# Kernel optimization log

Measured on AMD Instinct MI355X. Metric: run time of the kernel, lower is better.

## Reference

```python
import jax, jax.numpy as jnp
import numpy as np

B, S, DM, H, HD = 2, 4096, 768, 12, 64   # longformer-base-4096
W = 256    # one-sided attention window (attention_window=512)
NB = S // W
G = 16     # number of leading global-attention tokens ([CLS]+query)
OUT = 512  # hidden_dim of final fc


def setup_inputs() -> dict:
    key = jax.random.key(0)
    ks = jax.random.split(key, 11)
    def w(k, shape):
        return jax.random.normal(k, shape, jnp.float32) * 0.02
    z = lambda n: jnp.zeros((n,), jnp.float32)
    return {
        "x": jax.random.normal(ks[0], (B, S, DM), jnp.float32),
        "wq": w(ks[1], (DM, DM)), "bq": z(DM),
        "wk": w(ks[2], (DM, DM)), "bk": z(DM),
        "wv": w(ks[3], (DM, DM)), "bv": z(DM),
        "wqg": w(ks[4], (DM, DM)), "bqg": z(DM),
        "wkg": w(ks[5], (DM, DM)), "bkg": z(DM),
        "wvg": w(ks[6], (DM, DM)), "bvg": z(DM),
        "wo": w(ks[7], (DM, DM)), "bo": z(DM),
        "wp": w(ks[8], (DM, DM)), "bp": z(DM),
        "wfc": w(ks[9], (DM, OUT)), "bfc": z(OUT),
    }


def _longformer_forward(x, wq, bq, wk, bk, wv, bv, wqg, bqg, wkg, bkg,
                        wvg, bvg, wo, bo, wp, bp, wfc, bfc):
    scale = jnp.float32(1.0 / np.sqrt(HD))
    q = ((x @ wq + bq) * scale).reshape(B, S, H, HD)
    k = (x @ wk + bk).reshape(B, S, H, HD)
    v = (x @ wv + bv).reshape(B, S, H, HD)

    # --- sliding-window (banded) attention via overlapping key/value blocks ---
    kp = jnp.pad(k, ((0, 0), (W, W), (0, 0), (0, 0)))  # [B, S+2W, H, HD]
    vp = jnp.pad(v, ((0, 0), (W, W), (0, 0), (0, 0)))
    blk = jnp.arange(NB)[:, None] * W + jnp.arange(3 * W)[None, :]  # [NB,3W]
    kb = kp[:, blk]  # [B, NB, 3W, H, HD]
    vb = vp[:, blk]
    qb = q.reshape(B, NB, W, H, HD)
    sc_loc = jnp.einsum('bnqhd,bnkhd->bhnqk', qb, kb)  # [B,H,NB,W,3W]

    i = jnp.arange(W)[:, None]
    j = jnp.arange(3 * W)[None, :]
    band = (j >= i) & (j <= i + 2 * W)                       # |rel| <= W
    abs_k = (jnp.arange(NB)[:, None, None] - 1) * W + j[None]  # [NB,W,3W]
    # mask padding, out-of-band, and global keys (handled separately per HF)
    valid = band[None] & (abs_k >= 0) & (abs_k < S) & (abs_k >= G)
    sc_loc = jnp.where(valid[None, None], sc_loc, jnp.float32(-1e9))

    # every query also attends to the G global keys (regular k/v per HF)
    sc_glb = jnp.einsum('bqhd,bghd->bhqg', q, k[:, :G])  # [B,H,S,G]

    sc = jnp.concatenate([sc_glb, sc_loc.reshape(B, H, S, 3 * W)], axis=-1)
    p = jax.nn.softmax(sc, axis=-1)
    p_g, p_l = p[..., :G], p[..., G:]
    out = jnp.einsum('bhqg,bghd->bqhd', p_g, v[:, :G])
    out = out + jnp.einsum('bhnqk,bnkhd->bnqhd',
                           p_l.reshape(B, H, NB, W, 3 * W), vb).reshape(B, S, H, HD)

    # --- global queries: full attention with the dedicated global projections ---
    qg = ((x[:, :G] @ wqg + bqg) * scale).reshape(B, G, H, HD)
    kg = (x @ wkg + bkg).reshape(B, S, H, HD)
    vg = (x @ wvg + bvg).reshape(B, S, H, HD)
    pg = jax.nn.softmax(jnp.einsum('bghd,bshd->bhgs', qg, kg), axis=-1)
    out_g = jnp.einsum('bhgs,bshd->bghd', pg, vg)
    out = jnp.concatenate([out_g, out[:, G:]], axis=1)

    attn = out.reshape(B, S, DM) @ wo + bo
    pooled = jnp.tanh(attn[:, 0] @ wp + bp)  # HF pooler on [CLS]
    return pooled @ wfc + bfc                # final nn.Linear -> [B, OUT]


def reference(x, wq, bq, wk, bk, wv, bv, wqg, bqg, wkg, bkg, wvg, bvg,
              wo, bo, wp, bp, wfc, bfc):
    return _longformer_forward(x, wq, bq, wk, bk, wv, bv, wqg, bqg, wkg,
                               bkg, wvg, bvg, wo, bo, wp, bp, wfc, bfc)
```

## Files before the change

kernel.cpp:

```cpp
#include <hip/hip_runtime.h>
#include <hip/hip_bf16.h>

#define BB 2
#define SS 4096
#define DM 768
#define NH 12
#define OUTC 512
#define QSCALE 0.125f
#define NCHUNK 128
#define CS 32
#define JT 32

__device__ __forceinline__ float wave_sum64(float v) {
#pragma unroll
  for (int o = 32; o > 0; o >>= 1) v += __shfl_xor(v, o, 64);
  return v;
}

__global__ __launch_bounds__(256) void kA(const float* __restrict__ x,
    const float* __restrict__ wqg, const float* __restrict__ bqg,
    const float* __restrict__ wkg, const float* __restrict__ bkg,
    float* __restrict__ qw_ws, float* __restrict__ qb_ws,
    float* __restrict__ l_ws, float* __restrict__ xw_ws) {
  int h = blockIdx.x, b = blockIdx.y, js = blockIdx.z, t = threadIdx.x;
  __shared__ float x0[DM];
  __shared__ float red[4][64];
  __shared__ float qg0[64];
  for (int i = t; i < DM; i += 256) x0[i] = x[(size_t)b*SS*DM + i];
  for (int i = t; i < 384; i += 256)
    xw_ws[((size_t)b*NH + h)*DM + js*384 + i] = 0.f;
  if (js == 0 && t == 0) l_ws[b*NH + h] = 0.f;
  __syncthreads();
  int d = t & 63, g = t >> 6;
  float p = 0.f;
  for (int j = g*192; j < g*192 + 192; ++j)
    p += x0[j] * wqg[(size_t)j*DM + h*64 + d];
  red[g][d] = p;
  __syncthreads();
  if (t < 64)
    qg0[t] = (red[0][t] + red[1][t] + red[2][t] + red[3][t] + bqg[h*64 + t]) * QSCALE;
  __syncthreads();
  if (js == 0 && t == 0) {
    float qb = 0.f;
    for (int dd = 0; dd < 64; ++dd) qb += qg0[dd] * bkg[h*64 + dd];
    qb_ws[b*NH + h] = qb;
  }
  const float4* qg4 = (const float4*)qg0;
  for (int jj = t; jj < 384; jj += 256) {
    int j = js*384 + jj;
    const float4* wr = (const float4*)(wkg + (size_t)j*DM + h*64);
    float acc = 0.f;
#pragma unroll
    for (int q = 0; q < 16; ++q) {
      float4 wv = wr[q], qv = qg4[q];
      acc += wv.x*qv.x + wv.y*qv.y + wv.z*qv.z + wv.w*qv.w;
    }
    qw_ws[((size_t)b*NH + h)*DM + j] = acc;
  }
}

__global__ __launch_bounds__(256) void kB(const float* __restrict__ x,
    const float* __restrict__ qw_ws, const float* __restrict__ qb_ws,
    float* __restrict__ l_ws, float* __restrict__ xw_ws) {
  int chunk = blockIdx.x, b = blockIdx.y;
  int t = threadIdx.x, lane = t & 63, w = t >> 6;
  __shared__ alignas(16) float qw[NH*DM];
  __shared__ float qb[NH];
  __shared__ alignas(16) float pl[CS*NH];
  for (int i = t; i < NH*DM; i += 256) qw[i] = qw_ws[(size_t)b*NH*DM + i];
  if (t < NH) qb[t] = qb_ws[b*NH + t];
  __syncthreads();
  const size_t xbase = ((size_t)b*SS + chunk*CS) * DM;
  const float4* x4 = (const float4*)(x + xbase);
  const float4* qw4 = (const float4*)qw;
  float lacc = 0.f;

  for (int batch = 0; batch < 2; ++batch) {
    int sl = w*8 + batch*4;
    float acc[4][NH];
#pragma unroll
    for (int si = 0; si < 4; ++si)
#pragma unroll
      for (int hh = 0; hh < NH; ++hh) acc[si][hh] = 0.f;
#pragma unroll
    for (int k = 0; k < 3; ++k) {
      int jq = k*64 + lane;
      float4 xf[4];
#pragma unroll
      for (int si = 0; si < 4; ++si)
        xf[si] = x4[(size_t)(sl + si)*192 + jq];
#pragma unroll
      for (int hh = 0; hh < NH; ++hh) {
        float4 qv = qw4[hh*192 + jq];
#pragma unroll
        for (int si = 0; si < 4; ++si)
          acc[si][hh] += xf[si].x*qv.x + xf[si].y*qv.y + xf[si].z*qv.z + xf[si].w*qv.w;
      }
    }
    float preg = 0.f;
#pragma unroll
    for (int si = 0; si < 4; ++si)
#pragma unroll
      for (int hh = 0; hh < NH; ++hh) {
        float r = wave_sum64(acc[si][hh]);
        float pp = __expf(r + qb[hh]);
        if (lane == hh) lacc += pp;
        if (lane == si*NH + hh) preg = pp;
      }
    if (lane < 4*NH) pl[(sl + lane/NH)*NH + (lane % NH)] = preg;
  }
  if (lane < NH) atomicAdd(&l_ws[b*NH + lane], lacc);
  __syncthreads();

  float a2[NH][3];
#pragma unroll
  for (int hh = 0; hh < NH; ++hh)
#pragma unroll
    for (int i = 0; i < 3; ++i) a2[hh][i] = 0.f;
  for (int s = 0; s < CS; ++s) {
    float4 p0 = *(const float4*)(&pl[s*NH + 0]);
    float4 p1 = *(const float4*)(&pl[s*NH + 4]);
    float4 p2 = *(const float4*)(&pl[s*NH + 8]);
    float pv[NH] = {p0.x,p0.y,p0.z,p0.w, p1.x,p1.y,p1.z,p1.w, p2.x,p2.y,p2.z,p2.w};
    float xv[3];
#pragma unroll
    for (int i = 0; i < 3; ++i)
      xv[i] = x[xbase + (size_t)s*DM + t + 256*i];
#pragma unroll
    for (int hh = 0; hh < NH; ++hh)
#pragma unroll
      for (int i = 0; i < 3; ++i) a2[hh][i] += pv[hh]*xv[i];
  }
#pragma unroll
  for (int hh = 0; hh < NH; ++hh)
#pragma unroll
    for (int i = 0; i < 3; ++i)
      atomicAdd(&xw_ws[((size_t)b*NH + hh)*DM + t + 256*i], a2[hh][i]);
}

__global__ __launch_bounds__(256) void kE1(const float* __restrict__ xw_ws,
    const float* __restrict__ l_ws, const float* __restrict__ wvg,
    const float* __restrict__ bvg, float* __restrict__ out0_ws,
    float* __restrict__ zbuf) {
  int h = blockIdx.x, b = blockIdx.y, t = threadIdx.x;
  __shared__ float xws[DM];
  __shared__ float red[4][64];
  int bid = b*NH + h;
  if (t < 128) zbuf[bid*128 + t] = 0.f;
  float inv = 1.f / l_ws[b*NH + h];
  for (int i = 0; i < 3; ++i) {
    int j = t + 256*i;
    xws[j] = xw_ws[((size_t)b*NH + h)*DM + j] * inv;
  }
  __syncthreads();
  int ci = t & 63, g = t >> 6;
  float acc = 0.f;
  for (int j = g*192; j < g*192 + 192; ++j)
    acc += xws[j] * wvg[(size_t)j*DM + h*64 + ci];
  red[g][ci] = acc;
  __syncthreads();
  if (t < 64)
    out0_ws[b*DM + h*64 + t] =
        red[0][t] + red[1][t] + red[2][t] + red[3][t] + bvg[h*64 + t];
}

__global__ __launch_bounds__(192) void kT(const float* __restrict__ inraw,
    const float* __restrict__ bias, const float* __restrict__ W,
    float* __restrict__ outacc) {
  int jb = blockIdx.x, t = threadIdx.x;
  __shared__ float xs[2][DM/JT];
  const int JR = DM/JT;
  int j0 = jb*JR;
  if (t < 2*JR) {
    int bb = t / JR, jj = t % JR;
    float v = inraw[bb*DM + j0 + jj];
    if (bias) v += bias[j0 + jj];
    xs[bb][jj] = v;
  }
  __syncthreads();
  float4 a0 = {0,0,0,0}, a1 = {0,0,0,0};
  const float4* W4 = (const float4*)W;
#pragma unroll 4
  for (int jj = 0; jj < JR; ++jj) {
    float4 wv = W4[(size_t)(j0 + jj)*192 + t];
    float s0 = xs[0][jj], s1 = xs[1][jj];
    a0.x += s0*wv.x; a0.y += s0*wv.y; a0.z += s0*wv.z; a0.w += s0*wv.w;
    a1.x += s1*wv.x; a1.y += s1*wv.y; a1.z += s1*wv.z; a1.w += s1*wv.w;
  }
  int c = t*4;
  atomicAdd(&outacc[c+0], a0.x); atomicAdd(&outacc[c+1], a0.y);
  atomicAdd(&outacc[c+2], a0.z); atomicAdd(&outacc[c+3], a0.w);
  atomicAdd(&outacc[DM+c+0], a1.x); atomicAdd(&outacc[DM+c+1], a1.y);
  atomicAdd(&outacc[DM+c+2], a1.z); atomicAdd(&outacc[DM+c+3], a1.w);
}

__global__ __launch_bounds__(256) void kT3(const float* __restrict__ pooledraw,
    const float* __restrict__ bp, const float* __restrict__ wfc,
    const float* __restrict__ bfc, float* __restrict__ out) {
  int tile = blockIdx.x, b = blockIdx.y, t = threadIdx.x;
  __shared__ float pl[DM];
  __shared__ float red[4][64];
  for (int i = t; i < DM; i += 256) pl[i] = tanhf(pooledraw[b*DM + i] + bp[i]);
  __syncthreads();
  int ci = t & 63, g = t >> 6;
  int c = tile*64 + ci;
  float acc = 0.f;
  for (int j = g*192; j < g*192 + 192; ++j)
    acc += pl[j] * wfc[(size_t)j*OUTC + c];
  red[g][ci] = acc;
  __syncthreads();
  if (t < 64)
    out[(size_t)b*OUTC + tile*64 + t] =
        red[0][t] + red[1][t] + red[2][t] + red[3][t] + bfc[tile*64 + t];
}

extern "C" void kernel_launch(void* const* d_in, const int* in_sizes, int n_in,
                              void* d_out, int out_size, void* d_ws, size_t ws_size,
                              hipStream_t stream) {
  const float* x   = (const float*)d_in[0];
  const float* wqg = (const float*)d_in[7];
  const float* bqg = (const float*)d_in[8];
  const float* wkg = (const float*)d_in[9];
  const float* bkg = (const float*)d_in[10];
  const float* wvg = (const float*)d_in[11];
  const float* bvg = (const float*)d_in[12];
  const float* wo  = (const float*)d_in[13];
  const float* bo  = (const float*)d_in[14];
  const float* wp  = (const float*)d_in[15];
  const float* bp  = (const float*)d_in[16];
  const float* wfc = (const float*)d_in[17];
  const float* bfc = (const float*)d_in[18];

  float* ws        = (float*)d_ws;
  float* qw        = ws;
  float* qb        = ws + 18432;
  float* l         = ws + 18456;
  float* xw        = ws + 18480;
  float* out0      = ws + 36912;
  float* attnraw   = ws + 38448;
  float* pooledraw = ws + 39984;

  kA <<<dim3(NH, BB, 2),  256, 0, stream>>>(x, wqg, bqg, wkg, bkg, qw, qb, l, xw);
  kB <<<dim3(NCHUNK, BB), 256, 0, stream>>>(x, qw, qb, l, xw);
  kE1<<<dim3(NH, BB),     256, 0, stream>>>(xw, l, wvg, bvg, out0, attnraw);
  kT <<<dim3(JT),         192, 0, stream>>>(out0, nullptr, wo, attnraw);
  kT <<<dim3(JT),         192, 0, stream>>>(attnraw, bo, wp, pooledraw);
  kT3<<<dim3(8, BB),      256, 0, stream>>>(pooledraw, bp, wfc, bfc, (float*)d_out);
}
```

Measured before the change: 199.7 us.

## Split kB across head groups and vectorize small GEMV kernels with float4

The main kernel kB is split into four head groups of three heads each along a new grid dimension, so it launches four times as many blocks, each using less shared memory and fewer registers. The cost is that x is re-read once per head group. kA splits the wkg projection four ways instead of two. kA, kE1 and kT3 switch their GEMVs to float4 weight loads with a 16-way reduction, and kT doubles its block count and fully unrolls its loop. Together these aim to raise occupancy and parallelism in a launch-bound, low-occupancy pipeline.

```diff
diff --git a/kernel.cpp b/kernel.cpp
--- a/kernel.cpp
+++ b/kernel.cpp
@@ -9,7 +9,12 @@
 #define QSCALE 0.125f
 #define NCHUNK 128
 #define CS 32
-#define JT 32
+#define HPB 3
+#define HG  (NH/HPB)
+#define JSA 4
+#define JWA (DM/JSA)
+#define JT 64
+#define JR (DM/JT)
 
 __device__ __forceinline__ float wave_sum64(float v) {
 #pragma unroll
@@ -24,30 +29,47 @@
     float* __restrict__ l_ws, float* __restrict__ xw_ws) {
   int h = blockIdx.x, b = blockIdx.y, js = blockIdx.z, t = threadIdx.x;
   __shared__ float x0[DM];
-  __shared__ float red[4][64];
+  __shared__ float4 red4[16][16];
   __shared__ float qg0[64];
   for (int i = t; i < DM; i += 256) x0[i] = x[(size_t)b*SS*DM + i];
-  for (int i = t; i < 384; i += 256)
-    xw_ws[((size_t)b*NH + h)*DM + js*384 + i] = 0.f;
+  for (int i = t; i < JWA; i += 256)
+    xw_ws[((size_t)b*NH + h)*DM + js*JWA + i] = 0.f;
   if (js == 0 && t == 0) l_ws[b*NH + h] = 0.f;
   __syncthreads();
-  int d = t & 63, g = t >> 6;
-  float p = 0.f;
-  for (int j = g*192; j < g*192 + 192; ++j)
-    p += x0[j] * wqg[(size_t)j*DM + h*64 + d];
-  red[g][d] = p;
-  __syncthreads();
-  if (t < 64)
-    qg0[t] = (red[0][t] + red[1][t] + red[2][t] + red[3][t] + bqg[h*64 + t]) * QSCALE;
-  __syncthreads();
-  if (js == 0 && t == 0) {
-    float qb = 0.f;
-    for (int dd = 0; dd < 64; ++dd) qb += qg0[dd] * bkg[h*64 + dd];
-    qb_ws[b*NH + h] = qb;
+  {
+    int cq = t & 15, jg = t >> 4;
+    const float4* wq4 = (const float4*)wqg;
+    float4 a = {0.f, 0.f, 0.f, 0.f};
+#pragma unroll 8
+    for (int jo = 0; jo < 48; ++jo) {
+      int j = jg*48 + jo;
+      float xv = x0[j];
+      float4 wv = wq4[(size_t)j*(DM/4) + h*16 + cq];
+      a.x += xv*wv.x; a.y += xv*wv.y; a.z += xv*wv.z; a.w += xv*wv.w;
+    }
+    red4[jg][cq] = a;
+  }
+  __syncthreads();
+  if (t < 16) {
+    float4 a = {0.f, 0.f, 0.f, 0.f};
+#pragma unroll
+    for (int jg = 0; jg < 16; ++jg) {
+      float4 r = red4[jg][t];
+      a.x += r.x; a.y += r.y; a.z += r.z; a.w += r.w;
+    }
+    float4 bq = ((const float4*)(bqg + h*64))[t];
+    a.x = (a.x + bq.x)*QSCALE; a.y = (a.y + bq.y)*QSCALE;
+    a.z = (a.z + bq.z)*QSCALE; a.w = (a.w + bq.w)*QSCALE;
+    ((float4*)qg0)[t] = a;
+  }
+  __syncthreads();
+  if (js == 0 && t < 64) {
+    float v = wave_sum64(qg0[t] * bkg[h*64 + t]);
+    if (t == 0) qb_ws[b*NH + h] = v;
   }
   const float4* qg4 = (const float4*)qg0;
-  for (int jj = t; jj < 384; jj += 256) {
-    int j = js*384 + jj;
+  for (int jj = t; jj < JWA; jj += 256) {
+    int j = js*JWA + jj;
     const float4* wr = (const float4*)(wkg + (size_t)j*DM + h*64);
     float acc = 0.f;
 #pragma unroll
@@ -62,13 +84,13 @@
 __global__ __launch_bounds__(256) void kB(const float* __restrict__ x,
     const float* __restrict__ qw_ws, const float* __restrict__ qb_ws,
     float* __restrict__ l_ws, float* __restrict__ xw_ws) {
-  int chunk = blockIdx.x, b = blockIdx.y;
+  int chunk = blockIdx.x, b = blockIdx.y, h0 = blockIdx.z * HPB;
   int t = threadIdx.x, lane = t & 63, w = t >> 6;
-  __shared__ alignas(16) float qw[NH*DM];
-  __shared__ float qb[NH];
-  __shared__ alignas(16) float pl[CS*NH];
-  for (int i = t; i < NH*DM; i += 256) qw[i] = qw_ws[(size_t)b*NH*DM + i];
-  if (t < NH) qb[t] = qb_ws[b*NH + t];
+  __shared__ alignas(16) float qw[HPB*DM];
+  __shared__ float qb[HPB];
+  __shared__ alignas(16) float pl[CS*HPB];
+  for (int i = t; i < HPB*DM; i += 256) qw[i] = qw_ws[((size_t)b*NH + h0)*DM + i];
+  if (t < HPB) qb[t] = qb_ws[b*NH + h0 + t];
   __syncthreads();
   const size_t xbase = ((size_t)b*SS + chunk*CS) * DM;
   const float4* x4 = (const float4*)(x + xbase);
@@ -77,11 +99,11 @@
 
   for (int batch = 0; batch < 2; ++batch) {
     int sl = w*8 + batch*4;
-    float acc[4][NH];
+    float acc[4][HPB];
 #pragma unroll
     for (int si = 0; si < 4; ++si)
 #pragma unroll
-      for (int hh = 0; hh < NH; ++hh) acc[si][hh] = 0.f;
+      for (int hh = 0; hh < HPB; ++hh) acc[si][hh] = 0.f;
 #pragma unroll
     for (int k = 0; k < 3; ++k) {
       int jq = k*64 + lane;
@@ -90,7 +112,7 @@
       for (int si = 0; si < 4; ++si)
         xf[si] = x4[(size_t)(sl + si)*192 + jq];
 #pragma unroll
-      for (int hh = 0; hh < NH; ++hh) {
+      for (int hh = 0; hh < HPB; ++hh) {
         float4 qv = qw4[hh*192 + jq];
 #pragma unroll
         for (int si = 0; si < 4; ++si)
@@ -101,41 +123,40 @@
 #pragma unroll
     for (int si = 0; si < 4; ++si)
 #pragma unroll
-      for (int hh = 0; hh < NH; ++hh) {
+      for (int hh = 0; hh < HPB; ++hh) {
         float r = wave_sum64(acc[si][hh]);
         float pp = __expf(r + qb[hh]);
         if (lane == hh) lacc += pp;
-        if (lane == si*NH + hh) preg = pp;
+        if (lane == si*HPB + hh) preg = pp;
       }
-    if (lane < 4*NH) pl[(sl + lane/NH)*NH + (lane % NH)] = preg;
-  }
-  if (lane < NH) atomicAdd(&l_ws[b*NH + lane], lacc);
-  __syncthreads();
-
-  float a2[NH][3];
-#pragma unroll
-  for (int hh = 0; hh < NH; ++hh)
+    if (lane < 4*HPB) pl[(sl + lane/HPB)*HPB + (lane % HPB)] = preg;
+  }
+  if (lane < HPB) atomicAdd(&l_ws[b*NH + h0 + lane], lacc);
+  __syncthreads();
+
+  float a2[HPB][3];
+#pragma unroll
+  for (int hh = 0; hh < HPB; ++hh)
 #pragma unroll
     for (int i = 0; i < 3; ++i) a2[hh][i] = 0.f;
   for (int s = 0; s < CS; ++s) {
-    float4 p0 = *(const float4*)(&pl[s*NH + 0]);
-    float4 p1 = *(const float4*)(&pl[s*NH + 4]);
-    float4 p2 = *(const float4*)(&pl[s*NH + 8]);
-    float pv[NH] = {p0.x,p0.y,p0.z,p0.w, p1.x,p1.y,p1.z,p1.w, p2.x,p2.y,p2.z,p2.w};
+    float pv[HPB];
+#pragma unroll
+    for (int hh = 0; hh < HPB; ++hh) pv[hh] = pl[s*HPB + hh];
     float xv[3];
 #pragma unroll
     for (int i = 0; i < 3; ++i)
       xv[i] = x[xbase + (size_t)s*DM + t + 256*i];
 #pragma unroll
-    for (int hh = 0; hh < NH; ++hh)
+    for (int hh = 0; hh < HPB; ++hh)
 #pragma unroll
       for (int i = 0; i < 3; ++i) a2[hh][i] += pv[hh]*xv[i];
   }
 #pragma unroll
-  for (int hh = 0; hh < NH; ++hh)
+  for (int hh = 0; hh < HPB; ++hh)
 #pragma unroll
     for (int i = 0; i < 3; ++i)
-      atomicAdd(&xw_ws[((size_t)b*NH + hh)*DM + t + 256*i], a2[hh][i]);
+      atomicAdd(&xw_ws[((size_t)b*NH + h0 + hh)*DM + t + 256*i], a2[hh][i]);
 }
 
 __global__ __launch_bounds__(256) void kE1(const float* __restrict__ xw_ws,
@@ -144,32 +165,48 @@
     float* __restrict__ zbuf) {
   int h = blockIdx.x, b = blockIdx.y, t = threadIdx.x;
   __shared__ float xws[DM];
-  __shared__ float red[4][64];
+  __shared__ float4 red4[16][16];
   int bid = b*NH + h;
   if (t < 128) zbuf[bid*128 + t] = 0.f;
-  float inv = 1.f / l_ws[b*NH + h];
+  float inv = 1.f / l_ws[bid];
+#pragma unroll
   for (int i = 0; i < 3; ++i) {
     int j = t + 256*i;
     xws[j] = xw_ws[((size_t)b*NH + h)*DM + j] * inv;
   }
   __syncthreads();
-  int ci = t & 63, g = t >> 6;
-  float acc = 0.f;
-  for (int j = g*192; j < g*192 + 192; ++j)
-    acc += xws[j] * wvg[(size_t)j*DM + h*64 + ci];
-  red[g][ci] = acc;
-  __syncthreads();
-  if (t < 64)
-    out0_ws[b*DM + h*64 + t] =
-        red[0][t] + red[1][t] + red[2][t] + red[3][t] + bvg[h*64 + t];
+  {
+    int cq = t & 15, jg = t >> 4;
+    const float4* wv4 = (const float4*)wvg;
+    float4 a = {0.f, 0.f, 0.f, 0.f};
+#pragma unroll 8
+    for (int jo = 0; jo < 48; ++jo) {
+      int j = jg*48 + jo;
+      float xv = xws[j];
+      float4 wv = wv4[(size_t)j*(DM/4) + h*16 + cq];
+      a.x += xv*wv.x; a.y += xv*wv.y; a.z += xv*wv.z; a.w += xv*wv.w;
+    }
+    red4[jg][cq] = a;
+  }
+  __syncthreads();
+  if (t < 16) {
+    float4 a = {0.f, 0.f, 0.f, 0.f};
+#pragma unroll
+    for (int jg = 0; jg < 16; ++jg) {
+      float4 r = red4[jg][t];
+      a.x += r.x; a.y += r.y; a.z += r.z; a.w += r.w;
+    }
+    float4 bv = ((const float4*)(bvg + h*64))[t];
+    a.x += bv.x; a.y += bv.y; a.z += bv.z; a.w += bv.w;
+    ((float4*)(out0_ws + (size_t)b*DM + h*64))[t] = a;
+  }
 }
 
 __global__ __launch_bounds__(192) void kT(const float* __restrict__ inraw,
     const float* __restrict__ bias, const float* __restrict__ W,
     float* __restrict__ outacc) {
   int jb = blockIdx.x, t = threadIdx.x;
-  __shared__ float xs[2][DM/JT];
-  const int JR = DM/JT;
+  __shared__ float xs[2][JR];
   int j0 = jb*JR;
   if (t < 2*JR) {
     int bb = t / JR, jj = t % JR;
@@ -180,7 +217,7 @@
   __syncthreads();
   float4 a0 = {0,0,0,0}, a1 = {0,0,0,0};
   const float4* W4 = (const float4*)W;
-#pragma unroll 4
+#pragma unroll
   for (int jj = 0; jj < JR; ++jj) {
     float4 wv = W4[(size_t)(j0 + jj)*192 + t];
     float s0 = xs[0][jj], s1 = xs[1][jj];
@@ -198,20 +235,35 @@
     const float* __restrict__ bp, const float* __restrict__ wfc,
     const float* __restrict__ bfc, float* __restrict__ out) {
   int tile = blockIdx.x, b = blockIdx.y, t = threadIdx.x;
-  __shared__ float pl[DM];
-  __shared__ float red[4][64];
-  for (int i = t; i < DM; i += 256) pl[i] = tanhf(pooledraw[b*DM + i] + bp[i]);
-  __syncthreads();
-  int ci = t & 63, g = t >> 6;
-  int c = tile*64 + ci;
-  float acc = 0.f;
-  for (int j = g*192; j < g*192 + 192; ++j)
-    acc += pl[j] * wfc[(size_t)j*OUTC + c];
-  red[g][ci] = acc;
-  __syncthreads();
-  if (t < 64)
-    out[(size_t)b*OUTC + tile*64 + t] =
-        red[0][t] + red[1][t] + red[2][t] + red[3][t] + bfc[tile*64 + t];
+  __shared__ float pls[DM];
+  __shared__ float4 red4[16][16];
+  for (int i = t; i < DM; i += 256) pls[i] = tanhf(pooledraw[b*DM + i] + bp[i]);
+  __syncthreads();
+  {
+    int cq = t & 15, jg = t >> 4;
+    const float4* w4 = (const float4*)wfc;
+    float4 a = {0.f, 0.f, 0.f, 0.f};
+#pragma unroll 8
+    for (int jo = 0; jo < 48; ++jo) {
+      int j = jg*48 + jo;
+      float pv = pls[j];
+      float4 wv = w4[(size_t)j*(OUTC/4) + tile*16 + cq];
+      a.x += pv*wv.x; a.y += pv*wv.y; a.z += pv*wv.z; a.w += pv*wv.w;
+    }
+    red4[jg][cq] = a;
+  }
+  __syncthreads();
+  if (t < 16) {
+    float4 a = {0.f, 0.f, 0.f, 0.f};
+#pragma unroll
+    for (int jg = 0; jg < 16; ++jg) {
+      float4 r = red4[jg][t];
+      a.x += r.x; a.y += r.y; a.z += r.z; a.w += r.w;
+    }
+    float4 bf = ((const float4*)(bfc + tile*64))[t];
+    a.x += bf.x; a.y += bf.y; a.z += bf.z; a.w += bf.w;
+    ((float4*)(out + (size_t)b*OUTC + tile*64))[t] = a;
+  }
 }
 
 extern "C" void kernel_launch(void* const* d_in, const int* in_sizes, int n_in,
@@ -240,8 +292,8 @@
   float* attnraw   = ws + 38448;
   float* pooledraw = ws + 39984;
 
-  kA <<<dim3(NH, BB, 2),  256, 0, stream>>>(x, wqg, bqg, wkg, bkg, qw, qb, l, xw);
-  kB <<<dim3(NCHUNK, BB), 256, 0, stream>>>(x, qw, qb, l, xw);
+  kA <<<dim3(NH, BB, JSA), 256, 0, stream>>>(x, wqg, bqg, wkg, bkg, qw, qb, l, xw);
+  kB <<<dim3(NCHUNK, BB, HG), 256, 0, stream>>>(x, qw, qb, l, xw);
   kE1<<<dim3(NH, BB),     256, 0, stream>>>(xw, l, wvg, bvg, out0, attnraw);
   kT <<<dim3(JT),         192, 0, stream>>>(out0, nullptr, wo, attnraw);
   kT <<<dim3(JT),         192, 0, stream>>>(attnraw, bo, wp, pooledraw);
```

Result: faster. 192.1 us (-3.8%).
